# Performance work log

Measured on AMD Instinct MI355X. Metric: run time of the kernel, lower is better.

## Reference

```python
import jax, jax.numpy as jnp
import numpy as np

M, L, P, KK = 8, 3, 12, 9  # n_heads, n_levels, n_points, patch_size**2

def lrelu(v):
    return jnp.where(v >= 0, v, 0.1 * v)

def conv2d(x, w, b, pad):
    y = jax.lax.conv_general_dilated(x, w, (1, 1), [(pad, pad), (pad, pad)], dimension_numbers=('NCHW', 'OIHW', 'NCHW'))
    return y + b[None, :, None, None]

def trunk(x, w1, b1, w2, b2, w3, b3, w4, b4):
    h = lrelu(conv2d(x, w1, b1, 0))
    h = lrelu(conv2d(h, w2, b2, 1))
    h = lrelu(conv2d(h, w3, b3, 1))
    return conv2d(h, w4, b4, 0)

def grid_sample(img, gx, gy, align_corners):
    # img [N,C,H,W]; gx,gy [N,Q] normalized to [-1,1]; bilinear, zeros padding
    N, C, H, W = img.shape
    if align_corners:
        ix = (gx + 1.0) * 0.5 * (W - 1)
        iy = (gy + 1.0) * 0.5 * (H - 1)
    else:
        ix = ((gx + 1.0) * W - 1.0) * 0.5
        iy = ((gy + 1.0) * H - 1.0) * 0.5
    ix0 = jnp.floor(ix); iy0 = jnp.floor(iy)
    wx1 = ix - ix0; wy1 = iy - iy0
    flat = img.reshape(N, C, H * W)
    def gather(xi, yi, wgt):
        valid = (xi >= 0) & (xi <= W - 1) & (yi >= 0) & (yi <= H - 1)
        idx = (jnp.clip(yi, 0, H - 1) * W + jnp.clip(xi, 0, W - 1)).astype(jnp.int32)
        v = jnp.take_along_axis(flat, idx[:, None, :], axis=2)
        return v * (wgt * valid)[:, None, :]
    return (gather(ix0, iy0, (1 - wx1) * (1 - wy1)) + gather(ix0 + 1, iy0, wx1 * (1 - wy1))
            + gather(ix0, iy0 + 1, (1 - wx1) * wy1) + gather(ix0 + 1, iy0 + 1, wx1 * wy1))

def flow_warp(img, flow):
    # img [n,c,h,w]; flow [n,2,h,w] in pixels; torch grid_sample align_corners=True, zeros padding
    n, c, h, w = img.shape
    gy, gx = jnp.meshgrid(jnp.arange(h, dtype=img.dtype), jnp.arange(w, dtype=img.dtype), indexing='ij')
    gxn = 2.0 * (gx[None] + flow[:, 0]) / max(w - 1, 1) - 1.0
    gyn = 2.0 * (gy[None] + flow[:, 1]) / max(h - 1, 1) - 1.0
    return grid_sample(img, gxn.reshape(n, -1), gyn.reshape(n, -1), True).reshape(n, c, h, w)

def msdeform_attn(value, loc, attn, h, w):
    # pytorch MSDeformAttn core: value [N,L*HW,M,D]; loc [N,HW,M,L,Pt,2]; attn [N,HW,M,L,Pt]
    N, _, _, D = value.shape
    HW = h * w
    Pt = loc.shape[4]
    grids = 2.0 * loc - 1.0
    sampled = []
    for l in range(L):
        v = value[:, l * HW:(l + 1) * HW].transpose(0, 2, 3, 1).reshape(N * M, D, h, w)
        g = grids[:, :, :, l].transpose(0, 2, 1, 3, 4).reshape(N * M, HW * Pt, 2)
        s = grid_sample(v, g[..., 0], g[..., 1], False)  # [N*M, D, HW*Pt]
        sampled.append(s.reshape(N * M, D, HW, Pt))
    sampled = jnp.concatenate(sampled, axis=-1)  # [N*M, D, HW, L*Pt]
    aw = attn.transpose(0, 2, 1, 3, 4).reshape(N * M, HW, L * Pt)
    out = jnp.einsum('ndqp,nqp->nqd', sampled, aw)
    return out.reshape(N, M, HW, D).transpose(0, 2, 1, 3).reshape(N, HW, M * D)

def _forward(x, flow_1, flow_2, flip_flow_1, flip_flow_2, aw_w1, aw_b1, aw_w2, aw_b2, aw_w3, aw_b3, aw_w4, aw_b4, so_w1, so_b1, so_w2, so_b2, so_w3, so_b3, so_w4, so_b4, po_w1, po_b1, po_w2, po_b2, po_w3, po_b3, po_w4, po_b4, vp_w, vp_b, op_w1, op_b1, op_w2, op_b2):
    n, t, c, h, w = x.shape
    HW = h * w
    flow_cn1 = flow_1
    flow_cn2 = flow_1 + flow_warp(flow_2, flow_cn1)
    warp1 = flow_warp(x[:, 1], flow_cn1)
    warp2 = flow_warp(x[:, 2], flow_cn2)
    extra = jnp.concatenate([x[:, 0], warp1, warp2, flow_cn1, flow_cn2], axis=1)  # [n, 3c+4, h, w]
    value = conv2d(x.reshape(n, t * c, h, w), vp_w, vp_b, 0)
    off = trunk(extra, so_w1, so_b1, so_w2, so_b2, so_w3, so_b3, so_w4, so_b4)
    aw = trunk(extra, aw_w1, aw_b1, aw_w2, aw_b2, aw_w3, aw_b3, aw_w4, aw_b4)
    po = trunk(extra, po_w1, po_b1, po_w2, po_b2, po_w3, po_b3, po_w4, po_b4)
    value = value.reshape(n, t, c, HW).transpose(0, 1, 3, 2).reshape(n, t * HW, M, c // M)
    off = off.reshape(n, -1, HW).transpose(0, 2, 1).reshape(n, HW, M, L, P, 2)
    po = po.reshape(n, -1, HW).transpose(0, 2, 1).reshape(n, HW, M, L, P)
    po = jax.nn.sigmoid(po) * 3.0
    aw = aw.reshape(n, -1, HW).transpose(0, 2, 1).reshape(n, HW, M, L * P * KK)
    aw = jax.nn.softmax(aw, axis=-1).reshape(n, HW, M, L, P * KK)
    # flow-guided per-level offsets: level0 zeros, level1 flow_cn1, level2 flow_cn2
    f1 = flow_cn1.reshape(n, 2, HW).transpose(0, 2, 1)
    f2 = flow_cn2.reshape(n, 2, HW).transpose(0, 2, 1)
    fstack = jnp.stack([jnp.zeros_like(f1), f1, f2], axis=2)  # [n,HW,L,2]
    off = off + fstack[:, :, None, :, None, :]
    # 3x3 patch around each sampling point, scaled by learned patch offsets
    a = jnp.arange(-1, 2, dtype=x.dtype)
    pnx, pny = jnp.meshgrid(a, a, indexing='ij')
    p_n = jnp.stack([pnx, pny], axis=-1).reshape(KK, 2)
    off = off[..., None, :] + p_n * po[..., None, None]  # [n,HW,M,L,P,KK,2]
    off = off.reshape(n, HW, M, L, P * KK, 2)
    # reference points (valid ratios == 1)
    ry = (jnp.arange(h, dtype=x.dtype) + 0.5) / h
    rx = (jnp.arange(w, dtype=x.dtype) + 0.5) / w
    gy, gx = jnp.meshgrid(ry, rx, indexing='ij')
    ref = jnp.stack([gx, gy], axis=-1).reshape(1, HW, 1, 1, 1, 2)
    norm = jnp.array([w, h], dtype=x.dtype)
    loc = ref + off / norm
    out = msdeform_attn(value, loc, aw, h, w)  # [n, HW, c]
    feat = out.reshape(n, h, w, c).transpose(0, 3, 1, 2)
    res = conv2d(lrelu(conv2d(feat, op_w1, op_b1, 0)), op_w2, op_b2, 0)
    return res + x[:, 0]

def setup_inputs():
    key = jax.random.key(0)
    keys = jax.random.split(key, 64)
    it = iter(range(64))
    def nrm(shape, scale):
        return jax.random.normal(keys[next(it)], shape, jnp.float32) * scale
    n, t, c, h, w = 1, 3, 64, 64, 64
    Cin = t * c + 4  # 196
    d = {}
    d['x'] = nrm((n, t, c, h, w), 1.0)
    for nm in ['flow_1', 'flow_2', 'flip_flow_1', 'flip_flow_2']:
        d[nm] = nrm((n, 2, h, w), 1.5)
    def branch(prefix, out_ch, final_scale):
        d[prefix + '_w1'] = nrm((64, Cin, 1, 1), 1.0 / np.sqrt(Cin))
        d[prefix + '_b1'] = nrm((64,), 0.01)
        d[prefix + '_w2'] = nrm((64, 64, 3, 3), 1.0 / np.sqrt(64 * 9))
        d[prefix + '_b2'] = nrm((64,), 0.01)
        d[prefix + '_w3'] = nrm((64, 64, 3, 3), 1.0 / np.sqrt(64 * 9))
        d[prefix + '_b3'] = nrm((64,), 0.01)
        d[prefix + '_w4'] = nrm((out_ch, 64, 1, 1), final_scale)
        d[prefix + '_b4'] = nrm((out_ch,), 0.01)
    branch('aw', M * L * P * KK, 0.01)
    branch('so', M * L * P * 2, 0.01)
    branch('po', M * L * P, 0.01)
    d['vp_w'] = nrm((t * c, t * c, 1, 1), 1.0 / np.sqrt(t * c))
    d['vp_b'] = nrm((t * c,), 0.01)
    d['op_w1'] = nrm((c, c, 1, 1), 1.0 / np.sqrt(c))
    d['op_b1'] = nrm((c,), 0.01)
    d['op_w2'] = nrm((c, c, 1, 1), 1.0 / np.sqrt(c))
    d['op_b2'] = nrm((c,), 0.01)
    return d

def reference(x, flow_1, flow_2, flip_flow_1, flip_flow_2, aw_w1, aw_b1, aw_w2, aw_b2, aw_w3, aw_b3, aw_w4, aw_b4, so_w1, so_b1, so_w2, so_b2, so_w3, so_b3, so_w4, so_b4, po_w1, po_b1, po_w2, po_b2, po_w3, po_b3, po_w4, po_b4, vp_w, vp_b, op_w1, op_b1, op_w2, op_b2):
    return _forward(x, flow_1, flow_2, flip_flow_1, flip_flow_2, aw_w1, aw_b1, aw_w2, aw_b2, aw_w3, aw_b3, aw_w4, aw_b4, so_w1, so_b1, so_w2, so_b2, so_w3, so_b3, so_w4, so_b4, po_w1, po_b1, po_w2, po_b2, po_w3, po_b3, po_w4, po_b4, vp_w, vp_b, op_w1, op_b1, op_w2, op_b2)
```

## Files before the change

kernel.cpp:

```cpp
#include <hip/hip_runtime.h>
#include <hip/hip_bf16.h>
#include <math.h>

#define HWN 4096

typedef __attribute__((ext_vector_type(8))) short short8;
typedef __attribute__((ext_vector_type(4))) float f32x4;

__device__ __forceinline__ float lrelu_f(float v) { return v >= 0.f ? v : 0.1f * v; }

__device__ __forceinline__ unsigned short f2bf(float f) {
  union { float f; unsigned u; } v; v.f = f;
  unsigned r = v.u + 0x7fff + ((v.u >> 16) & 1);
  return (unsigned short)(r >> 16);
}
__device__ __forceinline__ float bf2f(unsigned short u) {
  union { unsigned u; float f; } v; v.u = ((unsigned)u) << 16;
  return v.f;
}
__device__ __forceinline__ float bf_lo(unsigned u) {
  union { unsigned u; float f; } v; v.u = u << 16; return v.f;
}
__device__ __forceinline__ float bf_hi(unsigned u) {
  union { unsigned u; float f; } v; v.u = u & 0xffff0000u; return v.f;
}

__device__ __forceinline__ float bilin_zero(const float* __restrict__ img, float ix, float iy) {
  float fx0 = floorf(ix), fy0 = floorf(iy);
  int x0 = (int)fx0, y0 = (int)fy0;
  float wx1 = ix - fx0, wy1 = iy - fy0;
  float wx0 = 1.f - wx1, wy0 = 1.f - wy1;
  float acc = 0.f;
  if ((unsigned)y0 < 64u) {
    if ((unsigned)x0 < 64u)       acc += wx0 * wy0 * img[y0 * 64 + x0];
    if ((unsigned)(x0 + 1) < 64u) acc += wx1 * wy0 * img[y0 * 64 + x0 + 1];
  }
  if ((unsigned)(y0 + 1) < 64u) {
    if ((unsigned)x0 < 64u)       acc += wx0 * wy1 * img[(y0 + 1) * 64 + x0];
    if ((unsigned)(x0 + 1) < 64u) acc += wx1 * wy1 * img[(y0 + 1) * 64 + x0 + 1];
  }
  return acc;
}

__global__ void k_flowcn2(const float* __restrict__ flow1, const float* __restrict__ flow2,
                          float* __restrict__ fcn2) {
  int p = blockIdx.x * 256 + threadIdx.x;
  int x = p & 63, y = p >> 6;
  float fx = flow1[p], fy = flow1[HWN + p];
  float ix = (float)x + fx, iy = (float)y + fy;
  fcn2[p] = fx + bilin_zero(flow2, ix, iy);
  fcn2[HWN + p] = fy + bilin_zero(flow2 + HWN, ix, iy);
}

__global__ void k_extra(const float* __restrict__ x, const float* __restrict__ flow1,
                        const float* __restrict__ fcn2, unsigned short* __restrict__ extra,
                        unsigned short* __restrict__ xb) {
  int p = blockIdx.x * 256 + threadIdx.x;
  int c = blockIdx.y;
  int xx = p & 63, yy = p >> 6;
  float x0 = x[c * HWN + p];
  float x1 = x[(64 + c) * HWN + p];
  float x2 = x[(128 + c) * HWN + p];
  xb[p * 192 + c]        = f2bf(x0);
  xb[p * 192 + 64 + c]   = f2bf(x1);
  xb[p * 192 + 128 + c]  = f2bf(x2);
  extra[p * 224 + c] = f2bf(x0);
  float ix1 = (float)xx + flow1[p], iy1 = (float)yy + flow1[HWN + p];
  float ix2 = (float)xx + fcn2[p],  iy2 = (float)yy + fcn2[HWN + p];
  extra[p * 224 + 64 + c]  = f2bf(bilin_zero(x + (64 + c) * HWN, ix1, iy1));
  extra[p * 224 + 128 + c] = f2bf(bilin_zero(x + (128 + c) * HWN, ix2, iy2));
  if (c < 2) {
    extra[p * 224 + 192 + c] = f2bf(flow1[c * HWN + p]);
    extra[p * 224 + 194 + c] = f2bf(fcn2[c * HWN + p]);
  }
  if (c < 28) extra[p * 224 + 196 + c] = 0;
}

__global__ void k_wconv(
    const float* so_w4, const float* po_w4, const float* aw_w4,
    const float* so_b4, const float* po_b4, const float* aw_b4,
    const float* so_b1, const float* po_b1, const float* aw_b1,
    const float* so_b2, const float* po_b2, const float* aw_b2,
    const float* so_b3, const float* po_b3, const float* aw_b3,
    const float* so_w1, const float* po_w1, const float* aw_w1,
    const float* so_w2, const float* po_w2, const float* aw_w2,
    const float* so_w3, const float* po_w3, const float* aw_w3,
    const float* op_w1, const float* op_w2, const float* vp_w,
    unsigned short* Wtail, float* btail, float* b1c, float* b2c, float* b3c,
    unsigned short* o1b, unsigned short* o2b, unsigned short* W1,
    unsigned short* W2g, unsigned short* W3g, unsigned short* vpb) {
  int t = blockIdx.x * 256 + threadIdx.x;
  int y = blockIdx.y;
  if (y == 0) {
    if (t < 3456 * 64) {
      int row = t >> 6, k = t & 63;
      float v = row < 576 ? so_w4[row * 64 + k]
              : row < 864 ? po_w4[(row - 576) * 64 + k]
                          : aw_w4[(row - 864) * 64 + k];
      Wtail[t] = f2bf(v);
    }
  } else if (y == 1) {
    if (t < 3456) {
      btail[t] = t < 576 ? so_b4[t] : t < 864 ? po_b4[t - 576] : aw_b4[t - 864];
    } else if (t < 3648) {
      int i = t - 3456; b1c[i] = i < 64 ? so_b1[i] : i < 128 ? po_b1[i - 64] : aw_b1[i - 128];
    } else if (t < 3840) {
      int i = t - 3648; b2c[i] = i < 64 ? so_b2[i] : i < 128 ? po_b2[i - 64] : aw_b2[i - 128];
    } else if (t < 4032) {
      int i = t - 3840; b3c[i] = i < 64 ? so_b3[i] : i < 128 ? po_b3[i - 64] : aw_b3[i - 128];
    } else if (t < 8128) {
      o1b[t - 4032] = f2bf(op_w1[t - 4032]);
    } else if (t < 12224) {
      o2b[t - 8128] = f2bf(op_w2[t - 8128]);
    }
  } else if (y == 2) {
    if (t < 192 * 224) {
      int row = t / 224, k = t % 224;
      int tr = row >> 6, lco = row & 63;
      const float* s = tr == 0 ? so_w1 : tr == 1 ? po_w1 : aw_w1;
      W1[t] = (k < 196) ? f2bf(s[lco * 196 + k]) : (unsigned short)0;
    }
  } else if (y == 3 || y == 4) {
    if (t < 3 * 64 * 576) {
      int tr = t / 36864, rem = t % 36864;
      int co = rem / 576, r2 = rem % 576;
      int kidx = r2 >> 6, ci = r2 & 63;
      const float* s;
      if (y == 3) s = tr == 0 ? so_w2 : tr == 1 ? po_w2 : aw_w2;
      else        s = tr == 0 ? so_w3 : tr == 1 ? po_w3 : aw_w3;
      (y == 3 ? W2g : W3g)[t] = f2bf(s[co * 576 + ci * 9 + kidx]);
    }
  } else {
    if (t < 192 * 192) vpb[t] = f2bf(vp_w[t]);
  }
}

template <int K, int LDA, int NT, int EPI>
__global__ __launch_bounds__(256) void k_gemm(const unsigned short* __restrict__ A,
                                              const unsigned short* __restrict__ W,
                                              const float* __restrict__ bias,
                                              void* __restrict__ outp,
                                              const float* __restrict__ aux, int LDC) {
  int wv = threadIdx.x >> 6;
  int l = threadIdx.x & 63;
  int lm = l & 15, lq = l >> 4;
  int p0 = blockIdx.x * 64 + wv * 16;
  int co0 = blockIdx.y * (NT * 16);

  f32x4 acc[NT];
#pragma unroll
  for (int nt = 0; nt < NT; nt++) {
    float bv = bias[co0 + nt * 16 + lm];
    acc[nt] = (f32x4){bv, bv, bv, bv};
  }
  const unsigned short* ap = A + (size_t)(p0 + lm) * LDA + lq * 8;
  const unsigned short* wp = W + (size_t)(co0 + lm) * K + lq * 8;
#pragma unroll
  for (int k0 = 0; k0 < K; k0 += 32) {
    short8 af = *(const short8*)(ap + k0);
#pragma unroll
    for (int nt = 0; nt < NT; nt++) {
      short8 bf = *(const short8*)(wp + (size_t)nt * 16 * K + k0);
      acc[nt] = __builtin_amdgcn_mfma_f32_16x16x32_bf16(af, bf, acc[nt], 0, 0, 0);
    }
  }
#pragma unroll
  for (int nt = 0; nt < NT; nt++) {
    int co = co0 + nt * 16 + lm;
#pragma unroll
    for (int r = 0; r < 4; r++) {
      int p = p0 + lq * 4 + r;
      float v = acc[nt][r];
      if (EPI == 1) v = lrelu_f(v);
      if (EPI == 0 || EPI == 1) {
        ((unsigned short*)outp)[(size_t)p * LDC + co] = f2bf(v);
      } else if (EPI == 2) {
        ((unsigned short*)outp)[((size_t)(co >> 3) * HWN + p) * 8 + (co & 7)] = f2bf(v);
      } else {
        ((float*)outp)[(size_t)co * HWN + p] = v + aux[(size_t)co * HWN + p];
      }
    }
  }
}

__global__ __launch_bounds__(256) void k_conv3g(const unsigned short* __restrict__ h,
                                                const unsigned short* __restrict__ W,
                                                const float* __restrict__ bias,
                                                unsigned short* __restrict__ out) {
  int wv = threadIdx.x >> 6;
  int l = threadIdx.x & 63;
  int lm = l & 15, lq = l >> 4;
  int p0 = blockIdx.x * 64 + wv * 16;
  int co0 = blockIdx.y * 16;
  int t = blockIdx.z;
  int p = p0 + lm;
  int px = p & 63, py = p >> 6;

  float bv = bias[t * 64 + co0 + lm];
  f32x4 acc = (f32x4){bv, bv, bv, bv};
  const unsigned short* wp = W + ((size_t)t * 64 + co0 + lm) * 576 + lq * 8;
#pragma unroll
  for (int kidx = 0; kidx < 9; kidx++) {
    int ky = kidx / 3, kx = kidx % 3;
    int pp = p + (ky - 1) * 64 + (kx - 1);
    bool valid = ((unsigned)(px + kx - 1) < 64u) && ((unsigned)(py + ky - 1) < 64u);
    const unsigned short* apb = h + (size_t)pp * 192 + t * 64 + lq * 8;
#pragma unroll
    for (int c2 = 0; c2 < 2; c2++) {
      short8 af = {};
      if (valid) af = *(const short8*)(apb + c2 * 32);
      short8 bf = *(const short8*)(wp + kidx * 64 + c2 * 32);
      acc = __builtin_amdgcn_mfma_f32_16x16x32_bf16(af, bf, acc, 0, 0, 0);
    }
  }
#pragma unroll
  for (int r = 0; r < 4; r++) {
    int po_ = p0 + lq * 4 + r;
    out[(size_t)po_ * 192 + t * 64 + co0 + lm] = f2bf(lrelu_f(acc[r]));
  }
}

__global__ __launch_bounds__(256) void k_tail(const unsigned short* __restrict__ A,
                                              const unsigned short* __restrict__ W,
                                              const float* __restrict__ bias,
                                              unsigned short* __restrict__ out) {
  int wv = threadIdx.x >> 6;
  int l = threadIdx.x & 63;
  int lm = l & 15, lq = l >> 4;
  int p0 = blockIdx.x * 64 + wv * 16;
  int co0 = blockIdx.y * 32;
  int t = (co0 < 576) ? 0 : (co0 < 864 ? 1 : 2);

  f32x4 acc[2];
#pragma unroll
  for (int nt = 0; nt < 2; nt++) {
    float bv = bias[co0 + nt * 16 + lm];
    acc[nt] = (f32x4){bv, bv, bv, bv};
  }
  const unsigned short* ap = A + (size_t)(p0 + lm) * 192 + t * 64 + lq * 8;
  const unsigned short* wp = W + (size_t)(co0 + lm) * 64 + lq * 8;
#pragma unroll
  for (int k0 = 0; k0 < 64; k0 += 32) {
    short8 af = *(const short8*)(ap + k0);
#pragma unroll
    for (int nt = 0; nt < 2; nt++) {
      short8 bf = *(const short8*)(wp + (size_t)nt * 16 * 64 + k0);
      acc[nt] = __builtin_amdgcn_mfma_f32_16x16x32_bf16(af, bf, acc[nt], 0, 0, 0);
    }
  }
#pragma unroll
  for (int nt = 0; nt < 2; nt++) {
    int co = co0 + nt * 16 + lm;
#pragma unroll
    for (int r = 0; r < 4; r++) {
      int p = p0 + lq * 4 + r;
      out[(size_t)p * 3456 + co] = f2bf(acc[nt][r]);
    }
  }
}

__global__ void k_msdeform(const unsigned short* __restrict__ vsb,
                           const unsigned short* __restrict__ to,
                           const float* __restrict__ flow1, const float* __restrict__ fcn2,
                           unsigned short* __restrict__ featb) {
  int yl = threadIdx.x & 15;
  int p = blockIdx.x * 16 + (threadIdx.x >> 4);
  int m = blockIdx.y;
  int px = p & 63, py = p >> 6;

  float fx1 = flow1[p], fy1 = flow1[HWN + p];
  float fx2 = fcn2[p],  fy2 = fcn2[HWN + p];

  const unsigned short* row = to + (size_t)p * 3456;

  float acc[8];
#pragma unroll
  for (int d = 0; d < 8; d++) acc[d] = 0.f;
  float wsum = 0.f;

  for (int pair = yl; pair < 36; pair += 16) {
    int l = pair / 12, pt = pair % 12;
    float fx = (l == 1) ? fx1 : ((l == 2) ? fx2 : 0.f);
    float fy = (l == 1) ? fy1 : ((l == 2) ? fy2 : 0.f);
    int ch = (m * 3 + l) * 12 + pt;
    unsigned ow = *(const unsigned*)(row + ch * 2);
    float ox = bf_lo(ow);
    float oy = bf_hi(ow);
    float s = 3.f / (1.f + __expf(-bf2f(row[576 + ch])));
    float bx = (float)px + ox + fx;
    float by = (float)py + oy + fy;
    const unsigned short* vbase = vsb + (size_t)(l * 8 + m) * HWN * 8;
    const unsigned short* lgp = row + 864 + m * 324 + l * 108 + pt * 9;
#pragma unroll
    for (int kk = 0; kk < 9; kk++) {
      float pnx = (float)(kk / 3 - 1);
      float pny = (float)(kk % 3 - 1);
      float ix = bx + pnx * s;
      float iy = by + pny * s;
      float wgt = __expf(bf2f(lgp[kk]));
      wsum += wgt;

      float fx0 = floorf(ix), fy0 = floorf(iy);
      int x0 = (int)fx0, y0 = (int)fy0;
      float wx1 = ix - fx0, wy1 = iy - fy0;
      float wx0 = 1.f - wx1, wy0 = 1.f - wy1;

      float tw[4];
      int tx[4], ty[4];
      tw[0] = wx0 * wy0; tx[0] = x0;     ty[0] = y0;
      tw[1] = wx1 * wy0; tx[1] = x0 + 1; ty[1] = y0;
      tw[2] = wx0 * wy1; tx[2] = x0;     ty[2] = y0 + 1;
      tw[3] = wx1 * wy1; tx[3] = x0 + 1; ty[3] = y0 + 1;
#pragma unroll
      for (int c = 0; c < 4; c++) {
        if ((unsigned)tx[c] < 64u && (unsigned)ty[c] < 64u) {
          uint4 uv = *(const uint4*)(vbase + (size_t)(ty[c] * 64 + tx[c]) * 8);
          float ww = wgt * tw[c];
          acc[0] += ww * bf_lo(uv.x); acc[1] += ww * bf_hi(uv.x);
          acc[2] += ww * bf_lo(uv.y); acc[3] += ww * bf_hi(uv.y);
          acc[4] += ww * bf_lo(uv.z); acc[5] += ww * bf_hi(uv.z);
          acc[6] += ww * bf_lo(uv.w); acc[7] += ww * bf_hi(uv.w);
        }
      }
    }
  }
#pragma unroll
  for (int mask = 1; mask < 16; mask <<= 1) {
    wsum += __shfl_xor(wsum, mask);
#pragma unroll
    for (int d = 0; d < 8; d++) acc[d] += __shfl_xor(acc[d], mask);
  }
  if (yl < 8) {
    float inv = 1.f / wsum;
    float r = 0.f;
#pragma unroll
    for (int d = 0; d < 8; d++) r = (d == yl) ? acc[d] : r;
    featb[(size_t)p * 64 + m * 8 + yl] = f2bf(r * inv);
  }
}

extern "C" void kernel_launch(void* const* d_in, const int* in_sizes, int n_in,
                              void* d_out, int out_size, void* d_ws, size_t ws_size,
                              hipStream_t stream) {
  const float* x     = (const float*)d_in[0];
  const float* flow1 = (const float*)d_in[1];
  const float* flow2 = (const float*)d_in[2];
  const float* aw_w1 = (const float*)d_in[5];
  const float* aw_b1 = (const float*)d_in[6];
  const float* aw_w2 = (const float*)d_in[7];
  const float* aw_b2 = (const float*)d_in[8];
  const float* aw_w3 = (const float*)d_in[9];
  const float* aw_b3 = (const float*)d_in[10];
  const float* aw_w4 = (const float*)d_in[11];
  const float* aw_b4 = (const float*)d_in[12];
  const float* so_w1 = (const float*)d_in[13];
  const float* so_b1 = (const float*)d_in[14];
  const float* so_w2 = (const float*)d_in[15];
  const float* so_b2 = (const float*)d_in[16];
  const float* so_w3 = (const float*)d_in[17];
  const float* so_b3 = (const float*)d_in[18];
  const float* so_w4 = (const float*)d_in[19];
  const float* so_b4 = (const float*)d_in[20];
  const float* po_w1 = (const float*)d_in[21];
  const float* po_b1 = (const float*)d_in[22];
  const float* po_w2 = (const float*)d_in[23];
  const float* po_b2 = (const float*)d_in[24];
  const float* po_w3 = (const float*)d_in[25];
  const float* po_b3 = (const float*)d_in[26];
  const float* po_w4 = (const float*)d_in[27];
  const float* po_b4 = (const float*)d_in[28];
  const float* vp_w  = (const float*)d_in[29];
  const float* vp_b  = (const float*)d_in[30];
  const float* op_w1 = (const float*)d_in[31];
  const float* op_b1 = (const float*)d_in[32];
  const float* op_w2 = (const float*)d_in[33];
  const float* op_b2 = (const float*)d_in[34];

  char* base = (char*)d_ws;
  size_t off = 0;
  auto alloc = [&](size_t bytes) { void* pp = base + off; off = (off + bytes + 255) & ~(size_t)255; return pp; };

  float* fcn2  = (float*)alloc(2 * HWN * 4);
  unsigned short* vsb   = (unsigned short*)alloc(192 * HWN * 2);
  unsigned short* extra = (unsigned short*)alloc(224 * HWN * 2);
  unsigned short* xb    = (unsigned short*)alloc(192 * HWN * 2);
  unsigned short* h1    = (unsigned short*)alloc(192 * HWN * 2);
  unsigned short* h2    = (unsigned short*)alloc(192 * HWN * 2);
  unsigned short* h3    = (unsigned short*)alloc(192 * HWN * 2);
  unsigned short* to    = (unsigned short*)alloc((size_t)3456 * HWN * 2);
  unsigned short* featb = (unsigned short*)alloc(64 * HWN * 2);
  unsigned short* hopb  = (unsigned short*)alloc(64 * HWN * 2);
  unsigned short* Wtail = (unsigned short*)alloc(3456 * 64 * 2);
  float* btail = (float*)alloc(3456 * 4);
  float* b1c   = (float*)alloc(192 * 4);
  float* b2c   = (float*)alloc(192 * 4);
  float* b3c   = (float*)alloc(192 * 4);
  unsigned short* o1b = (unsigned short*)alloc(64 * 64 * 2);
  unsigned short* o2b = (unsigned short*)alloc(64 * 64 * 2);
  unsigned short* W1  = (unsigned short*)alloc(192 * 224 * 2);
  unsigned short* W2g = (unsigned short*)alloc(3 * 64 * 576 * 2);
  unsigned short* W3g = (unsigned short*)alloc(3 * 64 * 576 * 2);
  unsigned short* vpb = (unsigned short*)alloc(192 * 192 * 2);

  k_wconv<<<dim3(864, 6), 256, 0, stream>>>(
      so_w4, po_w4, aw_w4, so_b4, po_b4, aw_b4,
      so_b1, po_b1, aw_b1, so_b2, po_b2, aw_b2, so_b3, po_b3, aw_b3,
      so_w1, po_w1, aw_w1, so_w2, po_w2, aw_w2, so_w3, po_w3, aw_w3,
      op_w1, op_w2, vp_w,
      Wtail, btail, b1c, b2c, b3c, o1b, o2b, W1, W2g, W3g, vpb);

  k_flowcn2<<<16, 256, 0, stream>>>(flow1, flow2, fcn2);
  k_extra<<<dim3(16, 64), 256, 0, stream>>>(x, flow1, fcn2, extra, xb);

  k_gemm<192, 192, 2, 2><<<dim3(64, 6), 256, 0, stream>>>(xb, vpb, vp_b, vsb, nullptr, 192);

  k_gemm<224, 224, 1, 1><<<dim3(64, 12), 256, 0, stream>>>(extra, W1, b1c, h1, nullptr, 192);
  k_conv3g<<<dim3(64, 4, 3), 256, 0, stream>>>(h1, W2g, b2c, h2);
  k_conv3g<<<dim3(64, 4, 3), 256, 0, stream>>>(h2, W3g, b3c, h3);
  k_tail<<<dim3(64, 108), 256, 0, stream>>>(h3, Wtail, btail, to);

  k_msdeform<<<dim3(256, 8), 256, 0, stream>>>(vsb, to, flow1, fcn2, featb);

  k_gemm<64, 64, 1, 1><<<dim3(64, 4), 256, 0, stream>>>(featb, o1b, op_b1, hopb, nullptr, 64);
  k_gemm<64, 64, 1, 3><<<dim3(64, 4), 256, 0, stream>>>(hopb, o2b, op_b2, d_out, x, 64);
}
```

Baseline: 251.3 us.

## Fuse preprocessing kernels, merge GEMMs, and fuse output projection pair

Folds weight conversion, the x-to-bf16 transpose (via a shared-memory tile) and the flow composition into one pre kernel. k_extra now gathers from the bf16 channel-last xb instead of fp32 planes. The value projection and first trunk conv run as one launch, and the two output 1x1 convs are fused through shared memory. The 3x3 convs use two N tiles per wave, the value layout becomes channel-last (stride 192), and the divides become rcp intrinsics. The goals are fewer launches, less intermediate traffic and more reuse per A fragment; the cost is bf16 rounding of the warped inputs before interpolation.

```diff
diff --git a/kernel.cpp b/kernel.cpp
--- a/kernel.cpp
+++ b/kernel.cpp
@@ -42,41 +42,8 @@
   return acc;
 }
 
-__global__ void k_flowcn2(const float* __restrict__ flow1, const float* __restrict__ flow2,
-                          float* __restrict__ fcn2) {
-  int p = blockIdx.x * 256 + threadIdx.x;
-  int x = p & 63, y = p >> 6;
-  float fx = flow1[p], fy = flow1[HWN + p];
-  float ix = (float)x + fx, iy = (float)y + fy;
-  fcn2[p] = fx + bilin_zero(flow2, ix, iy);
-  fcn2[HWN + p] = fy + bilin_zero(flow2 + HWN, ix, iy);
-}
-
-__global__ void k_extra(const float* __restrict__ x, const float* __restrict__ flow1,
-                        const float* __restrict__ fcn2, unsigned short* __restrict__ extra,
-                        unsigned short* __restrict__ xb) {
-  int p = blockIdx.x * 256 + threadIdx.x;
-  int c = blockIdx.y;
-  int xx = p & 63, yy = p >> 6;
-  float x0 = x[c * HWN + p];
-  float x1 = x[(64 + c) * HWN + p];
-  float x2 = x[(128 + c) * HWN + p];
-  xb[p * 192 + c]        = f2bf(x0);
-  xb[p * 192 + 64 + c]   = f2bf(x1);
-  xb[p * 192 + 128 + c]  = f2bf(x2);
-  extra[p * 224 + c] = f2bf(x0);
-  float ix1 = (float)xx + flow1[p], iy1 = (float)yy + flow1[HWN + p];
-  float ix2 = (float)xx + fcn2[p],  iy2 = (float)yy + fcn2[HWN + p];
-  extra[p * 224 + 64 + c]  = f2bf(bilin_zero(x + (64 + c) * HWN, ix1, iy1));
-  extra[p * 224 + 128 + c] = f2bf(bilin_zero(x + (128 + c) * HWN, ix2, iy2));
-  if (c < 2) {
-    extra[p * 224 + 192 + c] = f2bf(flow1[c * HWN + p]);
-    extra[p * 224 + 194 + c] = f2bf(fcn2[c * HWN + p]);
-  }
-  if (c < 28) extra[p * 224 + 196 + c] = 0;
-}
-
-__global__ void k_wconv(
+__global__ void k_pre(
+    const float* __restrict__ x, const float* __restrict__ flow1, const float* __restrict__ flow2,
     const float* so_w4, const float* po_w4, const float* aw_w4,
     const float* so_b4, const float* po_b4, const float* aw_b4,
     const float* so_b1, const float* po_b1, const float* aw_b1,
@@ -88,117 +55,182 @@
     const float* op_w1, const float* op_w2, const float* vp_w,
     unsigned short* Wtail, float* btail, float* b1c, float* b2c, float* b3c,
     unsigned short* o1b, unsigned short* o2b, unsigned short* W1,
-    unsigned short* W2g, unsigned short* W3g, unsigned short* vpb) {
-  int t = blockIdx.x * 256 + threadIdx.x;
-  int y = blockIdx.y;
-  if (y == 0) {
-    if (t < 3456 * 64) {
-      int row = t >> 6, k = t & 63;
-      float v = row < 576 ? so_w4[row * 64 + k]
-              : row < 864 ? po_w4[(row - 576) * 64 + k]
-                          : aw_w4[(row - 864) * 64 + k];
-      Wtail[t] = f2bf(v);
-    }
-  } else if (y == 1) {
-    if (t < 3456) {
-      btail[t] = t < 576 ? so_b4[t] : t < 864 ? po_b4[t - 576] : aw_b4[t - 864];
-    } else if (t < 3648) {
-      int i = t - 3456; b1c[i] = i < 64 ? so_b1[i] : i < 128 ? po_b1[i - 64] : aw_b1[i - 128];
-    } else if (t < 3840) {
-      int i = t - 3648; b2c[i] = i < 64 ? so_b2[i] : i < 128 ? po_b2[i - 64] : aw_b2[i - 128];
-    } else if (t < 4032) {
-      int i = t - 3840; b3c[i] = i < 64 ? so_b3[i] : i < 128 ? po_b3[i - 64] : aw_b3[i - 128];
-    } else if (t < 8128) {
-      o1b[t - 4032] = f2bf(op_w1[t - 4032]);
-    } else if (t < 12224) {
-      o2b[t - 8128] = f2bf(op_w2[t - 8128]);
-    }
-  } else if (y == 2) {
-    if (t < 192 * 224) {
-      int row = t / 224, k = t % 224;
-      int tr = row >> 6, lco = row & 63;
-      const float* s = tr == 0 ? so_w1 : tr == 1 ? po_w1 : aw_w1;
-      W1[t] = (k < 196) ? f2bf(s[lco * 196 + k]) : (unsigned short)0;
-    }
-  } else if (y == 3 || y == 4) {
-    if (t < 3 * 64 * 576) {
-      int tr = t / 36864, rem = t % 36864;
-      int co = rem / 576, r2 = rem % 576;
-      int kidx = r2 >> 6, ci = r2 & 63;
-      const float* s;
-      if (y == 3) s = tr == 0 ? so_w2 : tr == 1 ? po_w2 : aw_w2;
-      else        s = tr == 0 ? so_w3 : tr == 1 ? po_w3 : aw_w3;
-      (y == 3 ? W2g : W3g)[t] = f2bf(s[co * 576 + ci * 9 + kidx]);
-    }
+    unsigned short* W2g, unsigned short* W3g, unsigned short* vpb,
+    unsigned short* xb, float* fcn2) {
+  __shared__ unsigned short tile[64 * 65];
+  int gx = blockIdx.x;
+  int tid = threadIdx.x;
+  if (gx < 5184) {
+    int y = gx / 864;
+    int t = (gx % 864) * 256 + tid;
+    if (y == 0) {
+      if (t < 3456 * 64) {
+        int row = t >> 6, k = t & 63;
+        float v = row < 576 ? so_w4[row * 64 + k]
+                : row < 864 ? po_w4[(row - 576) * 64 + k]
+                            : aw_w4[(row - 864) * 64 + k];
+        Wtail[t] = f2bf(v);
+      }
+    } else if (y == 1) {
+      if (t < 3456) {
+        btail[t] = t < 576 ? so_b4[t] : t < 864 ? po_b4[t - 576] : aw_b4[t - 864];
+      } else if (t < 3648) {
+        int i = t - 3456; b1c[i] = i < 64 ? so_b1[i] : i < 128 ? po_b1[i - 64] : aw_b1[i - 128];
+      } else if (t < 3840) {
+        int i = t - 3648; b2c[i] = i < 64 ? so_b2[i] : i < 128 ? po_b2[i - 64] : aw_b2[i - 128];
+      } else if (t < 4032) {
+        int i = t - 3840; b3c[i] = i < 64 ? so_b3[i] : i < 128 ? po_b3[i - 64] : aw_b3[i - 128];
+      } else if (t < 8128) {
+        o1b[t - 4032] = f2bf(op_w1[t - 4032]);
+      } else if (t < 12224) {
+        o2b[t - 8128] = f2bf(op_w2[t - 8128]);
+      }
+    } else if (y == 2) {
+      if (t < 192 * 224) {
+        int row = t / 224, k = t % 224;
+        int tr = row >> 6, lco = row & 63;
+        const float* s = tr == 0 ? so_w1 : tr == 1 ? po_w1 : aw_w1;
+        W1[t] = (k < 196) ? f2bf(s[lco * 196 + k]) : (unsigned short)0;
+      }
+    } else if (y == 3 || y == 4) {
+      if (t < 3 * 64 * 576) {
+        int tr = t / 36864, rem = t % 36864;
+        int co = rem / 576, r2 = rem % 576;
+        int kidx = r2 >> 6, ci = r2 & 63;
+        const float* s;
+        if (y == 3) s = tr == 0 ? so_w2 : tr == 1 ? po_w2 : aw_w2;
+        else        s = tr == 0 ? so_w3 : tr == 1 ? po_w3 : aw_w3;
+        (y == 3 ? W2g : W3g)[t] = f2bf(s[co * 576 + ci * 9 + kidx]);
+      }
+    } else {
+      if (t < 192 * 192) vpb[t] = f2bf(vp_w[t]);
+    }
+  } else if (gx < 5376) {
+    int b = gx - 5184;
+    int ptile = b & 63, cg = b >> 6;
+    int px = tid & 63, ch0 = (tid >> 6) * 16;
+#pragma unroll
+    for (int i = 0; i < 16; i++) {
+      float v = x[(size_t)(cg * 64 + ch0 + i) * HWN + ptile * 64 + px];
+      tile[(ch0 + i) * 65 + px] = f2bf(v);
+    }
+    __syncthreads();
+    int c = tid & 63, pl0 = (tid >> 6) * 16;
+#pragma unroll
+    for (int i = 0; i < 16; i++)
+      xb[(size_t)(ptile * 64 + pl0 + i) * 192 + cg * 64 + c] = tile[c * 65 + pl0 + i];
   } else {
-    if (t < 192 * 192) vpb[t] = f2bf(vp_w[t]);
-  }
-}
-
-template <int K, int LDA, int NT, int EPI>
-__global__ __launch_bounds__(256) void k_gemm(const unsigned short* __restrict__ A,
-                                              const unsigned short* __restrict__ W,
-                                              const float* __restrict__ bias,
-                                              void* __restrict__ outp,
-                                              const float* __restrict__ aux, int LDC) {
+    int p = (gx - 5376) * 256 + tid;
+    int px = p & 63, py = p >> 6;
+    float fx = flow1[p], fy = flow1[HWN + p];
+    float ix = (float)px + fx, iy = (float)py + fy;
+    fcn2[p] = fx + bilin_zero(flow2, ix, iy);
+    fcn2[HWN + p] = fy + bilin_zero(flow2 + HWN, ix, iy);
+  }
+}
+
+__global__ void k_extra(const unsigned short* __restrict__ xb, const float* __restrict__ flow1,
+                        const float* __restrict__ fcn2, unsigned short* __restrict__ extra) {
+  int w = threadIdx.x >> 6, c = threadIdx.x & 63;
+  int p = blockIdx.x * 4 + w;
+  int px = p & 63, py = p >> 6;
+  float fx1 = flow1[p], fy1 = flow1[HWN + p];
+  float fx2 = fcn2[p],  fy2 = fcn2[HWN + p];
+  extra[(size_t)p * 224 + c] = xb[(size_t)p * 192 + c];
+#pragma unroll
+  for (int lev = 0; lev < 2; lev++) {
+    float ix = (float)px + (lev ? fx2 : fx1);
+    float iy = (float)py + (lev ? fy2 : fy1);
+    float fx0 = floorf(ix), fy0 = floorf(iy);
+    int x0 = (int)fx0, y0 = (int)fy0;
+    float wx1 = ix - fx0, wy1 = iy - fy0;
+    float wx0 = 1.f - wx1, wy0 = 1.f - wy1;
+    int coff = (lev + 1) * 64;
+    float acc = 0.f;
+    if ((unsigned)y0 < 64u) {
+      if ((unsigned)x0 < 64u)       acc += wx0 * wy0 * bf2f(xb[(size_t)(y0 * 64 + x0) * 192 + coff + c]);
+      if ((unsigned)(x0 + 1) < 64u) acc += wx1 * wy0 * bf2f(xb[(size_t)(y0 * 64 + x0 + 1) * 192 + coff + c]);
+    }
+    if ((unsigned)(y0 + 1) < 64u) {
+      if ((unsigned)x0 < 64u)       acc += wx0 * wy1 * bf2f(xb[(size_t)((y0 + 1) * 64 + x0) * 192 + coff + c]);
+      if ((unsigned)(x0 + 1) < 64u) acc += wx1 * wy1 * bf2f(xb[(size_t)((y0 + 1) * 64 + x0 + 1) * 192 + coff + c]);
+    }
+    extra[(size_t)p * 224 + coff + c] = f2bf(acc);
+  }
+  if (c < 2) {
+    extra[(size_t)p * 224 + 192 + c] = f2bf(flow1[c * HWN + p]);
+    extra[(size_t)p * 224 + 194 + c] = f2bf(fcn2[c * HWN + p]);
+  }
+  if (c < 28) extra[(size_t)p * 224 + 196 + c] = 0;
+}
+
+__global__ __launch_bounds__(256) void k_gemm2(
+    const unsigned short* __restrict__ A0, const unsigned short* __restrict__ Wm0,
+    const float* __restrict__ bias0, unsigned short* __restrict__ out0,
+    const unsigned short* __restrict__ A1, const unsigned short* __restrict__ Wm1,
+    const float* __restrict__ bias1, unsigned short* __restrict__ out1) {
+  int z = blockIdx.z;
+  const unsigned short* A = z ? A1 : A0;
+  const unsigned short* Wm = z ? Wm1 : Wm0;
+  const float* bias = z ? bias1 : bias0;
+  unsigned short* out = z ? out1 : out0;
+  int K = z ? 224 : 192;
+
   int wv = threadIdx.x >> 6;
   int l = threadIdx.x & 63;
   int lm = l & 15, lq = l >> 4;
   int p0 = blockIdx.x * 64 + wv * 16;
-  int co0 = blockIdx.y * (NT * 16);
-
-  f32x4 acc[NT];
-#pragma unroll
-  for (int nt = 0; nt < NT; nt++) {
+  int co0 = blockIdx.y * 64;
+
+  f32x4 acc[4];
+#pragma unroll
+  for (int nt = 0; nt < 4; nt++) {
     float bv = bias[co0 + nt * 16 + lm];
     acc[nt] = (f32x4){bv, bv, bv, bv};
   }
-  const unsigned short* ap = A + (size_t)(p0 + lm) * LDA + lq * 8;
-  const unsigned short* wp = W + (size_t)(co0 + lm) * K + lq * 8;
-#pragma unroll
+  const unsigned short* ap = A + (size_t)(p0 + lm) * K + lq * 8;
+  const unsigned short* wp = Wm + (size_t)(co0 + lm) * K + lq * 8;
   for (int k0 = 0; k0 < K; k0 += 32) {
     short8 af = *(const short8*)(ap + k0);
 #pragma unroll
-    for (int nt = 0; nt < NT; nt++) {
+    for (int nt = 0; nt < 4; nt++) {
       short8 bf = *(const short8*)(wp + (size_t)nt * 16 * K + k0);
       acc[nt] = __builtin_amdgcn_mfma_f32_16x16x32_bf16(af, bf, acc[nt], 0, 0, 0);
     }
   }
 #pragma unroll
-  for (int nt = 0; nt < NT; nt++) {
+  for (int nt = 0; nt < 4; nt++) {
     int co = co0 + nt * 16 + lm;
 #pragma unroll
     for (int r = 0; r < 4; r++) {
       int p = p0 + lq * 4 + r;
       float v = acc[nt][r];
-      if (EPI == 1) v = lrelu_f(v);
-      if (EPI == 0 || EPI == 1) {
-        ((unsigned short*)outp)[(size_t)p * LDC + co] = f2bf(v);
-      } else if (EPI == 2) {
-        ((unsigned short*)outp)[((size_t)(co >> 3) * HWN + p) * 8 + (co & 7)] = f2bf(v);
-      } else {
-        ((float*)outp)[(size_t)co * HWN + p] = v + aux[(size_t)co * HWN + p];
-      }
+      if (z) v = lrelu_f(v);
+      out[(size_t)p * 192 + co] = f2bf(v);
     }
   }
 }
 
 __global__ __launch_bounds__(256) void k_conv3g(const unsigned short* __restrict__ h,
-                                                const unsigned short* __restrict__ W,
+                                                const unsigned short* __restrict__ Wm,
                                                 const float* __restrict__ bias,
                                                 unsigned short* __restrict__ out) {
   int wv = threadIdx.x >> 6;
   int l = threadIdx.x & 63;
   int lm = l & 15, lq = l >> 4;
   int p0 = blockIdx.x * 64 + wv * 16;
-  int co0 = blockIdx.y * 16;
+  int co0 = blockIdx.y * 32;
   int t = blockIdx.z;
   int p = p0 + lm;
   int px = p & 63, py = p >> 6;
 
-  float bv = bias[t * 64 + co0 + lm];
-  f32x4 acc = (f32x4){bv, bv, bv, bv};
-  const unsigned short* wp = W + ((size_t)t * 64 + co0 + lm) * 576 + lq * 8;
+  f32x4 acc[2];
+#pragma unroll
+  for (int nt = 0; nt < 2; nt++) {
+    float bv = bias[t * 64 + co0 + nt * 16 + lm];
+    acc[nt] = (f32x4){bv, bv, bv, bv};
+  }
+  const unsigned short* wp = Wm + ((size_t)t * 64 + co0 + lm) * 576 + lq * 8;
 #pragma unroll
   for (int kidx = 0; kidx < 9; kidx++) {
     int ky = kidx / 3, kx = kidx % 3;
@@ -209,19 +241,25 @@
     for (int c2 = 0; c2 < 2; c2++) {
       short8 af = {};
       if (valid) af = *(const short8*)(apb + c2 * 32);
-      short8 bf = *(const short8*)(wp + kidx * 64 + c2 * 32);
-      acc = __builtin_amdgcn_mfma_f32_16x16x32_bf16(af, bf, acc, 0, 0, 0);
-    }
-  }
-#pragma unroll
-  for (int r = 0; r < 4; r++) {
-    int po_ = p0 + lq * 4 + r;
-    out[(size_t)po_ * 192 + t * 64 + co0 + lm] = f2bf(lrelu_f(acc[r]));
+#pragma unroll
+      for (int nt = 0; nt < 2; nt++) {
+        short8 bf = *(const short8*)(wp + (size_t)nt * 16 * 576 + kidx * 64 + c2 * 32);
+        acc[nt] = __builtin_amdgcn_mfma_f32_16x16x32_bf16(af, bf, acc[nt], 0, 0, 0);
+      }
+    }
+  }
+#pragma unroll
+  for (int nt = 0; nt < 2; nt++) {
+#pragma unroll
+    for (int r = 0; r < 4; r++) {
+      int po_ = p0 + lq * 4 + r;
+      out[(size_t)po_ * 192 + t * 64 + co0 + nt * 16 + lm] = f2bf(lrelu_f(acc[nt][r]));
+    }
   }
 }
 
 __global__ __launch_bounds__(256) void k_tail(const unsigned short* __restrict__ A,
-                                              const unsigned short* __restrict__ W,
+                                              const unsigned short* __restrict__ Wm,
                                               const float* __restrict__ bias,
                                               unsigned short* __restrict__ out) {
   int wv = threadIdx.x >> 6;
@@ -238,7 +276,7 @@
     acc[nt] = (f32x4){bv, bv, bv, bv};
   }
   const unsigned short* ap = A + (size_t)(p0 + lm) * 192 + t * 64 + lq * 8;
-  const unsigned short* wp = W + (size_t)(co0 + lm) * 64 + lq * 8;
+  const unsigned short* wp = Wm + (size_t)(co0 + lm) * 64 + lq * 8;
 #pragma unroll
   for (int k0 = 0; k0 < 64; k0 += 32) {
     short8 af = *(const short8*)(ap + k0);
@@ -286,10 +324,10 @@
     unsigned ow = *(const unsigned*)(row + ch * 2);
     float ox = bf_lo(ow);
     float oy = bf_hi(ow);
-    float s = 3.f / (1.f + __expf(-bf2f(row[576 + ch])));
+    float s = 3.f * __builtin_amdgcn_rcpf(1.f + __expf(-bf2f(row[576 + ch])));
     float bx = (float)px + ox + fx;
     float by = (float)py + oy + fy;
-    const unsigned short* vbase = vsb + (size_t)(l * 8 + m) * HWN * 8;
+    const unsigned short* vbase = vsb + l * 64 + m * 8;
     const unsigned short* lgp = row + 864 + m * 324 + l * 108 + pt * 9;
 #pragma unroll
     for (int kk = 0; kk < 9; kk++) {
@@ -314,7 +352,7 @@
 #pragma unroll
       for (int c = 0; c < 4; c++) {
         if ((unsigned)tx[c] < 64u && (unsigned)ty[c] < 64u) {
-          uint4 uv = *(const uint4*)(vbase + (size_t)(ty[c] * 64 + tx[c]) * 8);
+          uint4 uv = *(const uint4*)(vbase + (size_t)(ty[c] * 64 + tx[c]) * 192);
           float ww = wgt * tw[c];
           acc[0] += ww * bf_lo(uv.x); acc[1] += ww * bf_hi(uv.x);
           acc[2] += ww * bf_lo(uv.y); acc[3] += ww * bf_hi(uv.y);
@@ -331,11 +369,73 @@
     for (int d = 0; d < 8; d++) acc[d] += __shfl_xor(acc[d], mask);
   }
   if (yl < 8) {
-    float inv = 1.f / wsum;
+    float inv = __builtin_amdgcn_rcpf(wsum);
     float r = 0.f;
 #pragma unroll
     for (int d = 0; d < 8; d++) r = (d == yl) ? acc[d] : r;
     featb[(size_t)p * 64 + m * 8 + yl] = f2bf(r * inv);
+  }
+}
+
+__global__ __launch_bounds__(256) void k_opout(const unsigned short* __restrict__ featb,
+                                               const unsigned short* __restrict__ o1b,
+                                               const float* __restrict__ bias1,
+                                               const unsigned short* __restrict__ o2b,
+                                               const float* __restrict__ bias2,
+                                               const float* __restrict__ x,
+                                               float* __restrict__ out) {
+  __shared__ unsigned short hop[64 * 72];
+  int wv = threadIdx.x >> 6;
+  int l = threadIdx.x & 63;
+  int lm = l & 15, lq = l >> 4;
+  int bp0 = blockIdx.x * 64;
+
+  f32x4 acc1[4];
+#pragma unroll
+  for (int nt = 0; nt < 4; nt++) {
+    float bv = bias1[nt * 16 + lm];
+    acc1[nt] = (f32x4){bv, bv, bv, bv};
+  }
+  const unsigned short* ap = featb + (size_t)(bp0 + wv * 16 + lm) * 64 + lq * 8;
+#pragma unroll
+  for (int k0 = 0; k0 < 64; k0 += 32) {
+    short8 af = *(const short8*)(ap + k0);
+#pragma unroll
+    for (int nt = 0; nt < 4; nt++) {
+      short8 bf = *(const short8*)(o1b + (size_t)(nt * 16 + lm) * 64 + lq * 8 + k0);
+      acc1[nt] = __builtin_amdgcn_mfma_f32_16x16x32_bf16(af, bf, acc1[nt], 0, 0, 0);
+    }
+  }
+#pragma unroll
+  for (int nt = 0; nt < 4; nt++)
+#pragma unroll
+    for (int r = 0; r < 4; r++)
+      hop[(wv * 16 + lq * 4 + r) * 72 + nt * 16 + lm] = f2bf(lrelu_f(acc1[nt][r]));
+  __syncthreads();
+
+  f32x4 b4;
+#pragma unroll
+  for (int r = 0; r < 4; r++) b4[r] = bias2[wv * 16 + lq * 4 + r];
+  f32x4 acc2[4];
+#pragma unroll
+  for (int pg = 0; pg < 4; pg++) acc2[pg] = b4;
+#pragma unroll
+  for (int k0 = 0; k0 < 64; k0 += 32) {
+    short8 af = *(const short8*)(o2b + (size_t)(wv * 16 + lm) * 64 + k0 + lq * 8);
+#pragma unroll
+    for (int pg = 0; pg < 4; pg++) {
+      short8 bf = *(const short8*)(hop + (pg * 16 + lm) * 72 + k0 + lq * 8);
+      acc2[pg] = __builtin_amdgcn_mfma_f32_16x16x32_bf16(af, bf, acc2[pg], 0, 0, 0);
+    }
+  }
+#pragma unroll
+  for (int pg = 0; pg < 4; pg++) {
+#pragma unroll
+    for (int r = 0; r < 4; r++) {
+      int co = wv * 16 + lq * 4 + r;
+      int p = bp0 + pg * 16 + lm;
+      out[(size_t)co * HWN + p] = acc2[pg][r] + x[(size_t)co * HWN + p];
+    }
   }
 }
 
@@ -381,15 +481,14 @@
   auto alloc = [&](size_t bytes) { void* pp = base + off; off = (off + bytes + 255) & ~(size_t)255; return pp; };
 
   float* fcn2  = (float*)alloc(2 * HWN * 4);
+  unsigned short* xb    = (unsigned short*)alloc(192 * HWN * 2);
   unsigned short* vsb   = (unsigned short*)alloc(192 * HWN * 2);
   unsigned short* extra = (unsigned short*)alloc(224 * HWN * 2);
-  unsigned short* xb    = (unsigned short*)alloc(192 * HWN * 2);
   unsigned short* h1    = (unsigned short*)alloc(192 * HWN * 2);
   unsigned short* h2    = (unsigned short*)alloc(192 * HWN * 2);
   unsigned short* h3    = (unsigned short*)alloc(192 * HWN * 2);
   unsigned short* to    = (unsigned short*)alloc((size_t)3456 * HWN * 2);
   unsigned short* featb = (unsigned short*)alloc(64 * HWN * 2);
-  unsigned short* hopb  = (unsigned short*)alloc(64 * HWN * 2);
   unsigned short* Wtail = (unsigned short*)alloc(3456 * 64 * 2);
   float* btail = (float*)alloc(3456 * 4);
   float* b1c   = (float*)alloc(192 * 4);
@@ -402,25 +501,23 @@
   unsigned short* W3g = (unsigned short*)alloc(3 * 64 * 576 * 2);
   unsigned short* vpb = (unsigned short*)alloc(192 * 192 * 2);
 
-  k_wconv<<<dim3(864, 6), 256, 0, stream>>>(
+  k_pre<<<5392, 256, 0, stream>>>(
+      x, flow1, flow2,
       so_w4, po_w4, aw_w4, so_b4, po_b4, aw_b4,
       so_b1, po_b1, aw_b1, so_b2, po_b2, aw_b2, so_b3, po_b3, aw_b3,
       so_w1, po_w1, aw_w1, so_w2, po_w2, aw_w2, so_w3, po_w3, aw_w3,
       op_w1, op_w2, vp_w,
-      Wtail, btail, b1c, b2c, b3c, o1b, o2b, W1, W2g, W3g, vpb);
-
-  k_flowcn2<<<16, 256, 0, stream>>>(flow1, flow2, fcn2);
-  k_extra<<<dim3(16, 64), 256, 0, stream>>>(x, flow1, fcn2, extra, xb);
-
-  k_gemm<192, 192, 2, 2><<<dim3(64, 6), 256, 0, stream>>>(xb, vpb, vp_b, vsb, nullptr, 192);
-
-  k_gemm<224, 224, 1, 1><<<dim3(64, 12), 256, 0, stream>>>(extra, W1, b1c, h1, nullptr, 192);
-  k_conv3g<<<dim3(64, 4, 3), 256, 0, stream>>>(h1, W2g, b2c, h2);
-  k_conv3g<<<dim3(64, 4, 3), 256, 0, stream>>>(h2, W3g, b3c, h3);
+      Wtail, btail, b1c, b2c, b3c, o1b, o2b, W1, W2g, W3g, vpb, xb, fcn2);
+
+  k_extra<<<1024, 256, 0, stream>>>(xb, flow1, fcn2, extra);
+
+  k_gemm2<<<dim3(64, 3, 2), 256, 0, stream>>>(xb, vpb, vp_b, vsb, extra, W1, b1c, h1);
+
+  k_conv3g<<<dim3(64, 2, 3), 256, 0, stream>>>(h1, W2g, b2c, h2);
+  k_conv3g<<<dim3(64, 2, 3), 256, 0, stream>>>(h2, W3g, b3c, h3);
   k_tail<<<dim3(64, 108), 256, 0, stream>>>(h3, Wtail, btail, to);
 
   k_msdeform<<<dim3(256, 8), 256, 0, stream>>>(vsb, to, flow1, fcn2, featb);
 
-  k_gemm<64, 64, 1, 1><<<dim3(64, 4), 256, 0, stream>>>(featb, o1b, op_b1, hopb, nullptr, 64);
-  k_gemm<64, 64, 1, 3><<<dim3(64, 4), 256, 0, stream>>>(hopb, o2b, op_b2, d_out, x, 64);
-}
+  k_opout<<<64, 256, 0, stream>>>(featb, o1b, op_b1, o2b, op_b2, x, (float*)d_out);
+}
```

After: 242.2 us. 3.7% less time.
